# Kernel optimization log

Hardware: AMD Instinct MI355X
Metric: run time of the kernel (lower is better)

Reference implementation:

```python
import jax, jax.numpy as jnp
import numpy as np

B, M, N, D = 16, 1024, 1024, 512
DIST_THRESH = 0.3
NUM_SINK = 8


def setup_inputs() -> dict:
    key = jax.random.key(0)
    k1, k2, k3, k4 = jax.random.split(key, 4)
    return {
        "tra_feats": jax.random.normal(k1, (B, M, D), jnp.float32),
        "det_feats": jax.random.normal(k2, (B, N, D), jnp.float32),
        "tra_loc": jax.random.uniform(k3, (B, M, 2), jnp.float32),
        "det_loc": jax.random.uniform(k4, (B, N, 2), jnp.float32),
        "alpha": jnp.ones((1,), jnp.float32),
        "eplison": jnp.zeros((1,), jnp.float32),
    }


def _sinkhorn(C, log_a, log_b, lambd, num_sink):
    # log-domain unrolled Sinkhorn: P_ij = exp(log_p), marginals a (rows), b (cols)
    log_p = -C / lambd
    def step(lp, _):
        lp = lp - (jax.nn.logsumexp(lp, axis=-1, keepdims=True) - log_a[:, None])
        lp = lp - (jax.nn.logsumexp(lp, axis=-2, keepdims=True) - log_b[None, :])
        return lp, None
    log_p, _ = jax.lax.scan(step, log_p, None, length=num_sink)
    # final row normalization (standard unrolled-sinkhorn convention)
    log_p = log_p - (jax.nn.logsumexp(log_p, axis=-1, keepdims=True) - log_a[:, None])
    return jnp.exp(log_p)


def _per_graph(tf, df, tl, dl, alpha, lambd):
    n1 = jnp.linalg.norm(tf, axis=-1, keepdims=True)          # [M,1]
    n2 = jnp.linalg.norm(df, axis=-1, keepdims=True)          # [N,1]
    d2 = jnp.sum((tl[:, None, :] - dl[None, :, :]) ** 2, -1)  # [M,N] squared cdist
    mask = (jnp.sqrt(d2) <= DIST_THRESH).astype(tf.dtype)
    corr = (tf @ df.T) / (n1 * n2.T) * mask                   # masked cosine similarity
    m, n = corr.shape
    # augment with dustbin row/col filled with learnable alpha
    top = jnp.concatenate([corr, jnp.full((m, 1), alpha, corr.dtype)], axis=1)
    bot = jnp.full((1, n + 1), alpha, corr.dtype)
    couplings = jnp.concatenate([top, bot], axis=0)           # [M+1, N+1]
    norm = 1.0 / (m + n)
    a_aug = jnp.full((m + 1,), norm, corr.dtype).at[-1].set(norm * n)
    b_aug = jnp.full((n + 1,), norm, corr.dtype).at[-1].set(norm * m)
    p = _sinkhorn(1.0 - couplings, jnp.log(a_aug), jnp.log(b_aug), lambd, NUM_SINK)
    return p * (m + n)


def reference(tra_feats, det_feats, tra_loc, det_loc, alpha, eplison):
    a = alpha[0]
    lambd = jnp.exp(eplison[0]) + 0.03
    f = jax.vmap(lambda tf, df, tl, dl: _per_graph(tf, df, tl, dl, a, lambd))
    return f(tra_feats, det_feats, tra_loc, det_loc)   # [B, M+1, N+1]
```

## Files before the change

### kernel.cpp

```cpp
#include <hip/hip_runtime.h>
#include <math.h>

#define B_ 16
#define M_ 1024
#define N_ 1024
#define D_ 512
#define MP1 1025
#define NP1 1025
#define NUM_SINK 8
#define BK 64
#define SSTR 1024
#define VSTR 1028
#define NCHK 16
#define LOG_NORM (-7.6246189861593985f)
#define LOG_HALF (-0.6931471805599453f)

typedef __attribute__((ext_vector_type(8))) short bf16x8;
typedef __attribute__((ext_vector_type(4))) float f32x4;
typedef __attribute__((ext_vector_type(2))) float f32x2;

__device__ inline short f2bf(float x) {
    unsigned u = __builtin_bit_cast(unsigned, x);
    u = (u + 0x7FFFu + ((u >> 16) & 1u)) >> 16;
    return (short)u;
}

#if __has_builtin(__builtin_amdgcn_cvt_pk_fp8_f32) && __has_builtin(__builtin_amdgcn_cvt_pk_f32_fp8)
#define FP8_HW 1
#else
#define FP8_HW 0
#endif

__device__ inline unsigned char enc8(float x) {
#if FP8_HW
    return (unsigned char)(__builtin_amdgcn_cvt_pk_fp8_f32(x, x, 0, false) & 0xFF);
#else
    unsigned s = (__builtin_bit_cast(unsigned, x) >> 31) << 7;
    float ax = fminf(fabsf(x), 448.0f);
    unsigned bits;
    if (ax < 0.015625f) {
        bits = (unsigned)(ax * 512.0f + 0.5f);
        if (bits > 8) bits = 8;
    } else {
        int e; float m = frexpf(ax, &e);
        int k = e - 1;
        int j = (int)((m * 2.0f - 1.0f) * 8.0f + 0.5f);
        if (j == 8) { j = 0; k += 1; }
        if (k > 8) { k = 8; j = 7; }
        bits = ((unsigned)(k + 7) << 3) | (unsigned)j;
    }
    return (unsigned char)(s | bits);
#endif
}

__device__ inline void dec4(unsigned u, float* o) {
#if FP8_HW
    f32x2 a = __builtin_amdgcn_cvt_pk_f32_fp8((int)u, false);
    f32x2 b = __builtin_amdgcn_cvt_pk_f32_fp8((int)u, true);
    o[0] = a[0]; o[1] = a[1]; o[2] = b[0]; o[3] = b[1];
#else
    #pragma unroll
    for (int i = 0; i < 4; ++i) {
        unsigned bt = (u >> (8 * i)) & 0xFF;
        unsigned s = bt >> 7, em = bt & 0x7F;
        float mag;
        if (em >= 0x08) {
            unsigned fb = (((em >> 3) + 120) << 23) | ((em & 7) << 20);
            mag = __builtin_bit_cast(float, fb);
        } else {
            mag = (float)em * 0.001953125f;
        }
        o[i] = s ? -mag : mag;
    }
#endif
}

__device__ inline void gload16(const void* g, void* l) {
    __builtin_amdgcn_global_load_lds(
        (const __attribute__((address_space(1))) unsigned int*)g,
        (__attribute__((address_space(3))) unsigned int*)l, 16, 0, 0);
}

template<bool PRE>
__global__ __launch_bounds__(256) void norms_kernel_t(
    const float* __restrict__ tf, const float* __restrict__ df,
    float* __restrict__ inv1, float* __restrict__ inv2,
    unsigned short* __restrict__ tfh, unsigned short* __restrict__ dfh,
    float* __restrict__ v, float* __restrict__ sums_p)
{
    if (PRE && blockIdx.x == 0) {
        const int nv = B_ * VSTR, ns = 2 * B_ * 17;
        for (int t = threadIdx.x; t < nv + ns; t += 256) {
            if (t < nv) v[t] = 0.f;
            else {
                int u2 = t - nv;
                int p = u2 / (B_ * 17), s = u2 % 17;
                sums_p[u2] = (p == 0 && s == 0) ? 1025.0f : 0.f;
            }
        }
    }
    int w = (blockIdx.x * 256 + threadIdx.x) >> 6;
    int lane = threadIdx.x & 63;
    if (w >= B_ * 2048) return;
    int b = w >> 11;
    int rr = w & 2047;
    const float* src;
    float* dst = nullptr;
    unsigned short* dsth = nullptr;
    if (rr < M_) { src = tf + ((size_t)b * M_ + rr) * D_;
                   if (!PRE) dst = inv1 + b * M_ + rr;
                   if (PRE)  dsth = tfh + ((size_t)b * M_ + rr) * D_; }
    else         { src = df + ((size_t)b * N_ + (rr - M_)) * D_;
                   if (!PRE) dst = inv2 + b * N_ + (rr - M_);
                   if (PRE)  dsth = dfh + ((size_t)b * N_ + (rr - M_)) * D_; }
    float4 x = *(const float4*)(src + lane * 4);
    float4 y = *(const float4*)(src + 256 + lane * 4);
    float ss = x.x*x.x + x.y*x.y + x.z*x.z + x.w*x.w
             + y.x*y.x + y.y*y.y + y.z*y.z + y.w*y.w;
    #pragma unroll
    for (int o = 32; o; o >>= 1) ss += __shfl_xor(ss, o);
    if (PRE) {
        float rn = rsqrtf(ss);
        ushort4 hx, hy;
        hx.x = (unsigned short)f2bf(x.x*rn); hx.y = (unsigned short)f2bf(x.y*rn);
        hx.z = (unsigned short)f2bf(x.z*rn); hx.w = (unsigned short)f2bf(x.w*rn);
        hy.x = (unsigned short)f2bf(y.x*rn); hy.y = (unsigned short)f2bf(y.y*rn);
        hy.z = (unsigned short)f2bf(y.z*rn); hy.w = (unsigned short)f2bf(y.w*rn);
        *(ushort4*)(dsth + lane * 4) = hx;
        *(ushort4*)(dsth + 256 + lane * 4) = hy;
    } else {
        if (lane == 0) *dst = 1.0f / sqrtf(ss);
    }
}

template<int MODE>
__global__ __launch_bounds__(256) void gemm_s_kernel(
    const void* __restrict__ A, const void* __restrict__ Bm,
    const float* __restrict__ tl, const float* __restrict__ dl,
    const float* __restrict__ inv1, const float* __restrict__ inv2,
    const float* __restrict__ eps_p, void* __restrict__ Sout)
{
    __shared__ __align__(16) unsigned short As[2][128 * BK];
    __shared__ __align__(16) unsigned short Bs[2][128 * BK];

    int flat = blockIdx.x;
    int swz = (flat & 7) * 128 + (flat >> 3);
    int jb = swz & 7, ib = (swz >> 3) & 7;
    int b  = swz >> 6;
    int i0 = ib * 128;
    int j0 = jb * 128;

    int tid  = threadIdx.x;
    int lane = tid & 63;
    int w    = tid >> 6;
    int wm   = w >> 1, wn = w & 1;

    f32x4 acc[4][4] = {};

    if constexpr (MODE == 2) {
        const unsigned short* Ah = (const unsigned short*)A  + (size_t)b * M_ * D_;
        const unsigned short* Bh = (const unsigned short*)Bm + (size_t)b * N_ * D_;
        int gcol = ((lane & 7) ^ (lane >> 3)) << 3;
        int rloc = lane >> 3;

        auto stage = [&](int k0, int buf) {
            #pragma unroll
            for (int c = 0; c < 4; ++c) {
                int r = (w * 4 + c) * 8 + rloc;
                gload16(Ah + (size_t)(i0 + r) * D_ + k0 + gcol,
                        (char*)As[buf] + (w * 4 + c) * 1024 + lane * 16);
                gload16(Bh + (size_t)(j0 + r) * D_ + k0 + gcol,
                        (char*)Bs[buf] + (w * 4 + c) * 1024 + lane * 16);
            }
        };

        stage(0, 0);
        __syncthreads();
        int cur = 0;
        for (int t = 0; t < D_ / BK; ++t) {
            if (t < D_ / BK - 1) stage((t + 1) * BK, cur ^ 1);
            #pragma unroll
            for (int ks = 0; ks < 2; ++ks) {
                int kb = ks * 64 + ((lane >> 4) << 4);
                bf16x8 af[4], bfr[4];
                #pragma unroll
                for (int m = 0; m < 4; ++m) {
                    int ra = wm * 64 + m * 16 + (lane & 15);
                    af[m] = *(const bf16x8*)((const char*)As[cur] + ra * 128 + (kb ^ ((ra & 7) << 4)));
                    int rb = wn * 64 + m * 16 + (lane & 15);
                    bfr[m] = *(const bf16x8*)((const char*)Bs[cur] + rb * 128 + (kb ^ ((rb & 7) << 4)));
                }
                #pragma unroll
                for (int m = 0; m < 4; ++m)
                    #pragma unroll
                    for (int n = 0; n < 4; ++n)
                        acc[m][n] = __builtin_amdgcn_mfma_f32_16x16x32_bf16(af[m], bfr[n], acc[m][n], 0, 0, 0);
            }
            __syncthreads();
            cur ^= 1;
        }
    } else {
        const float* Ab = (const float*)A  + (size_t)b * M_ * D_;
        const float* Bb = (const float*)Bm + (size_t)b * N_ * D_;
        int seg   = tid & 7;
        int rbase = tid >> 3;
        for (int k0 = 0; k0 < D_; k0 += BK) {
            #pragma unroll
            for (int rr = 0; rr < 4; ++rr) {
                int r = rbase + rr * 32;
                int colx = (seg * 16) ^ ((r & 7) << 4);
                {
                    const float* pa = Ab + (size_t)(i0 + r) * D_ + k0 + seg * 8;
                    float4 a0 = *(const float4*)pa;
                    float4 a1 = *(const float4*)(pa + 4);
                    bf16x8 hv;
                    hv[0] = f2bf(a0.x); hv[1] = f2bf(a0.y); hv[2] = f2bf(a0.z); hv[3] = f2bf(a0.w);
                    hv[4] = f2bf(a1.x); hv[5] = f2bf(a1.y); hv[6] = f2bf(a1.z); hv[7] = f2bf(a1.w);
                    *(bf16x8*)((char*)As[0] + r * 128 + colx) = hv;
                }
                {
                    const float* pb = Bb + (size_t)(j0 + r) * D_ + k0 + seg * 8;
                    float4 b0 = *(const float4*)pb;
                    float4 b1 = *(const float4*)(pb + 4);
                    bf16x8 hv;
                    hv[0] = f2bf(b0.x); hv[1] = f2bf(b0.y); hv[2] = f2bf(b0.z); hv[3] = f2bf(b0.w);
                    hv[4] = f2bf(b1.x); hv[5] = f2bf(b1.y); hv[6] = f2bf(b1.z); hv[7] = f2bf(b1.w);
                    *(bf16x8*)((char*)Bs[0] + r * 128 + colx) = hv;
                }
            }
            __syncthreads();
            #pragma unroll
            for (int ks = 0; ks < 2; ++ks) {
                int kb = ks * 64 + ((lane >> 4) << 4);
                bf16x8 af[4], bfr[4];
                #pragma unroll
                for (int m = 0; m < 4; ++m) {
                    int ra = wm * 64 + m * 16 + (lane & 15);
                    af[m] = *(const bf16x8*)((const char*)As[0] + ra * 128 + (kb ^ ((ra & 7) << 4)));
                    int rb = wn * 64 + m * 16 + (lane & 15);
                    bfr[m] = *(const bf16x8*)((const char*)Bs[0] + rb * 128 + (kb ^ ((rb & 7) << 4)));
                }
                #pragma unroll
                for (int m = 0; m < 4; ++m)
                    #pragma unroll
                    for (int n = 0; n < 4; ++n)
                        acc[m][n] = __builtin_amdgcn_mfma_f32_16x16x32_bf16(af[m], bfr[n], acc[m][n], 0, 0, 0);
            }
            __syncthreads();
        }
    }

    float lam = __expf(eps_p[0]) + 0.03f;
    float inv_lam = 1.0f / lam;
    int crow0 = i0 + wm * 64;
    int ccol0 = j0 + wn * 64;
    int rlane = lane >> 4;
    int clane = lane & 15;

    float invb_[4], dlx_[4], dly_[4];
    #pragma unroll
    for (int n = 0; n < 4; ++n) {
        int j = ccol0 + n * 16 + clane;
        if (MODE != 2) invb_[n] = inv2[b * N_ + j];
        dlx_[n]  = dl[((size_t)b * N_ + j) * 2 + 0];
        dly_[n]  = dl[((size_t)b * N_ + j) * 2 + 1];
    }
    #pragma unroll
    for (int m = 0; m < 4; ++m) {
        #pragma unroll
        for (int reg = 0; reg < 4; ++reg) {
            int i = crow0 + m * 16 + rlane * 4 + reg;
            float inva = (MODE != 2) ? inv1[b * M_ + i] : 1.0f;
            float tlx  = tl[((size_t)b * M_ + i) * 2 + 0];
            float tly  = tl[((size_t)b * M_ + i) * 2 + 1];
            #pragma unroll
            for (int n = 0; n < 4; ++n) {
                float cosv = (MODE == 2) ? acc[m][n][reg]
                                         : acc[m][n][reg] * inva * invb_[n];
                float dx = tlx - dlx_[n];
                float dy = tly - dly_[n];
                float mi = (fmaf(dx, dx, dy * dy) <= 0.09f) ? inv_lam : 0.0f;
                float val = fmaf(cosv, mi, -inv_lam);
                int col = ccol0 + n * 16 + clane;
                if (MODE >= 1) {
                    unsigned char* Srow = (unsigned char*)Sout + ((size_t)b * M_ + i) * SSTR;
                    Srow[col] = enc8(val);
                } else {
                    float* Srow = (float*)Sout + ((size_t)b * MP1 + i) * NP1;
                    Srow[col] = val;
                }
            }
        }
    }
}

__global__ __launch_bounds__(256) void init_hv(
    float* __restrict__ v, float* __restrict__ sums_p)
{
    int t = blockIdx.x * 256 + threadIdx.x;
    if (t < B_ * VSTR) v[t] = 0.f;
    int u2 = t - B_ * VSTR;
    if (u2 >= 0 && u2 < 2 * B_ * 17) {
        int p = u2 / (B_ * 17), s = u2 % 17;
        sums_p[u2] = (p == 0 && s == 0) ? 1025.0f : 0.f;
    }
}

__global__ __launch_bounds__(256, 1) void rowcol64(
    const unsigned char* __restrict__ Sh, const float* __restrict__ v,
    float* __restrict__ ps,
    const float* __restrict__ alpha_p, const float* __restrict__ eps_p)
{
    int blk = blockIdx.x;
    int b = blk >> 4, k = blk & 15;
    int tid = threadIdx.x, lane = tid & 63, w = tid >> 6;

    __shared__ float red[4][64][17];

    const float* vb = v + (size_t)b * VSTR;
    float vreg[16];
    {
        float4 v0 = *(const float4*)(vb + lane * 8);
        float4 v1 = *(const float4*)(vb + lane * 8 + 4);
        float4 v2 = *(const float4*)(vb + 512 + lane * 8);
        float4 v3 = *(const float4*)(vb + 512 + lane * 8 + 4);
        vreg[0]=v0.x; vreg[1]=v0.y; vreg[2]=v0.z; vreg[3]=v0.w;
        vreg[4]=v1.x; vreg[5]=v1.y; vreg[6]=v1.z; vreg[7]=v1.w;
        vreg[8]=v2.x; vreg[9]=v2.y; vreg[10]=v2.z; vreg[11]=v2.w;
        vreg[12]=v3.x; vreg[13]=v3.y; vreg[14]=v3.z; vreg[15]=v3.w;
    }
    float lam = __expf(eps_p[0]) + 0.03f;
    float s_a = (alpha_p[0] - 1.0f) / lam;
    float et16c = __expf(s_a + vb[1024]);

    const unsigned char* Sb = Sh + ((size_t)b << 20);
    int rbase = k * 64 + w * 16;

    uint2 g0[16], g1[16];
    #pragma unroll
    for (int rr = 0; rr < 16; ++rr) {
        const unsigned char* row = Sb + (size_t)(rbase + rr) * SSTR;
        g0[rr] = *(const uint2*)(row + lane * 8);
        g1[rr] = *(const uint2*)(row + 512 + lane * 8);
    }

    float creg[16] = {};
    float sum_scale = 0.f;

    #pragma unroll
    for (int rr = 0; rr < 16; ++rr) {
        float d0[8], d1[8];
        dec4(g0[rr].x, d0); dec4(g0[rr].y, d0 + 4);
        dec4(g1[rr].x, d1); dec4(g1[rr].y, d1 + 4);
        float et[16];
        float rs = 0.f;
        #pragma unroll
        for (int e = 0; e < 8; ++e) { et[e] = __expf(d0[e] + vreg[e]); rs += et[e]; }
        #pragma unroll
        for (int e = 0; e < 8; ++e) { et[8+e] = __expf(d1[e] + vreg[8+e]); rs += et[8+e]; }
        #pragma unroll
        for (int o = 32; o; o >>= 1) rs += __shfl_xor(rs, o);
        rs += et16c;
        float scale = (1.0f / 2048.0f) / rs;
        #pragma unroll
        for (int e = 0; e < 16; ++e) creg[e] += et[e] * scale;
        sum_scale += scale;
    }

    #pragma unroll
    for (int e = 0; e < 16; ++e) red[w][lane][e] = creg[e];
    if (lane == 0) red[w][0][16] = sum_scale;
    __syncthreads();

    float* pso = ps + (size_t)(k * 16 + b) * 1025;
    for (int j = tid; j < 1024; j += 256) {
        int lane_j = (j & 511) >> 3;
        int e_j    = ((j >> 9) << 3) | (j & 7);
        pso[j] = red[0][lane_j][e_j] + red[1][lane_j][e_j]
               + red[2][lane_j][e_j] + red[3][lane_j][e_j];
    }
    if (tid == 0)
        pso[1024] = et16c * (red[0][0][16] + red[1][0][16] + red[2][0][16] + red[3][0][16]);
}

__global__ __launch_bounds__(256) void colpass32(
    const float* __restrict__ ps, float* __restrict__ v,
    float* __restrict__ sums_p, int it)
{
    int gw = blockIdx.x * 4 + (threadIdx.x >> 6);
    int lane = threadIdx.x & 63;
    if (gw >= B_ * 17) return;
    int b = gw / 17, seg = gw % 17;
    int j = seg * 64 + lane;
    int par = it & 1;
    float sum_old = 0.f;
    #pragma unroll
    for (int s = 0; s < 17; ++s) sum_old += sums_p[par * (B_ * 17) + b * 17 + s];
    float ev = 0.f;
    if (j <= 1024) {
        size_t vidx = (size_t)b * VSTR + j;
        float vj = v[vidx];
        const float* pp = ps + (size_t)b * 1025 + j;
        float cs = 0.f;
        #pragma unroll
        for (int c = 0; c < NCHK; ++c) cs += pp[(size_t)c * (16 * 1025)];
        cs += 0.5f * __expf(vj) / sum_old;
        float lb = (j == 1024) ? LOG_HALF : LOG_NORM;
        float vn = vj + lb - __logf(cs);
        v[vidx] = vn;
        ev = __expf(vn);
    }
    #pragma unroll
    for (int o = 32; o; o >>= 1) ev += __shfl_xor(ev, o);
    if (lane == 0) sums_p[(par ^ 1) * (B_ * 17) + b * 17 + seg] = ev;
}

__global__ __launch_bounds__(256) void final32(
    const unsigned char* __restrict__ Sh, const float* __restrict__ v,
    const float* __restrict__ sums_p,
    const float* __restrict__ alpha_p, const float* __restrict__ eps_p,
    float* __restrict__ out)
{
    int blk = blockIdx.x;
    int tid = threadIdx.x, lane = tid & 63, w = tid >> 6;

    if (blk >= 512) {
        int gw = (blk - 512) * 4 + w;
        if (gw >= B_ * 17) return;
        int b = gw / 17, seg = gw % 17, j = seg * 64 + lane;
        if (j > 1024) return;
        float sumv = 0.f;
        int par = NUM_SINK & 1;
        #pragma unroll
        for (int s = 0; s < 17; ++s) sumv += sums_p[par * (B_ * 17) + b * 17 + s];
        out[((size_t)b * MP1 + 1024) * NP1 + j] = __expf(v[(size_t)b * VSTR + j]) * 1024.0f / sumv;
        return;
    }

    int b = blk >> 5, k = blk & 31;
    const float* vb = v + (size_t)b * VSTR;
    float vreg[16];
    {
        float4 v0 = *(const float4*)(vb + lane * 8);
        float4 v1 = *(const float4*)(vb + lane * 8 + 4);
        float4 v2 = *(const float4*)(vb + 512 + lane * 8);
        float4 v3 = *(const float4*)(vb + 512 + lane * 8 + 4);
        vreg[0]=v0.x; vreg[1]=v0.y; vreg[2]=v0.z; vreg[3]=v0.w;
        vreg[4]=v1.x; vreg[5]=v1.y; vreg[6]=v1.z; vreg[7]=v1.w;
        vreg[8]=v2.x; vreg[9]=v2.y; vreg[10]=v2.z; vreg[11]=v2.w;
        vreg[12]=v3.x; vreg[13]=v3.y; vreg[14]=v3.z; vreg[15]=v3.w;
    }
    float lam = __expf(eps_p[0]) + 0.03f;
    float s_a = (alpha_p[0] - 1.0f) / lam;
    float et16c = __expf(s_a + vb[1024]);

    const unsigned char* Sb = Sh + ((size_t)b << 20);
    int rbase = k * 32 + w * 8;

    #pragma unroll
    for (int g = 0; g < 2; ++g) {
        uint2 g0[4], g1[4];
        #pragma unroll
        for (int rr = 0; rr < 4; ++rr) {
            const unsigned char* row = Sb + (size_t)(rbase + g * 4 + rr) * SSTR;
            g0[rr] = *(const uint2*)(row + lane * 8);
            g1[rr] = *(const uint2*)(row + 512 + lane * 8);
        }
        #pragma unroll
        for (int rr = 0; rr < 4; ++rr) {
            int r = rbase + g * 4 + rr;
            float d0[8], d1[8];
            dec4(g0[rr].x, d0); dec4(g0[rr].y, d0 + 4);
            dec4(g1[rr].x, d1); dec4(g1[rr].y, d1 + 4);
            float et[16];
            float rs = 0.f;
            #pragma unroll
            for (int e = 0; e < 8; ++e) { et[e] = __expf(d0[e] + vreg[e]); rs += et[e]; }
            #pragma unroll
            for (int e = 0; e < 8; ++e) { et[8+e] = __expf(d1[e] + vreg[8+e]); rs += et[8+e]; }
            #pragma unroll
            for (int o = 32; o; o >>= 1) rs += __shfl_xor(rs, o);
            rs += et16c;
            float sc = 1.0f / rs;
            float* orow = out + ((size_t)b * MP1 + r) * NP1;
            float4 o0 = {et[0]*sc,  et[1]*sc,  et[2]*sc,  et[3]*sc};
            float4 o1 = {et[4]*sc,  et[5]*sc,  et[6]*sc,  et[7]*sc};
            float4 o2 = {et[8]*sc,  et[9]*sc,  et[10]*sc, et[11]*sc};
            float4 o3 = {et[12]*sc, et[13]*sc, et[14]*sc, et[15]*sc};
            *(float4*)(orow + lane * 8)           = o0;
            *(float4*)(orow + lane * 8 + 4)       = o1;
            *(float4*)(orow + 512 + lane * 8)     = o2;
            *(float4*)(orow + 512 + lane * 8 + 4) = o3;
            if (lane == 0) orow[1024] = et16c * sc;
        }
    }
}


__global__ __launch_bounds__(256) void fill_edges_f32(
    float* __restrict__ Sout, const float* __restrict__ alpha_p, const float* __restrict__ eps_p)
{
    int t = blockIdx.x * 256 + threadIdx.x;
    if (t >= B_ * (NP1 + M_)) return;
    int b = t / (NP1 + M_), r = t % (NP1 + M_);
    float lam = expf(eps_p[0]) + 0.03f;
    float s = (alpha_p[0] - 1.0f) / lam;
    size_t idx;
    if (r < NP1) idx = ((size_t)b * MP1 + M_) * NP1 + r;
    else         idx = ((size_t)b * MP1 + (r - NP1)) * NP1 + N_;
    Sout[idx] = s;
}

__global__ __launch_bounds__(256) void row_pass_kernel(
    const float* __restrict__ S, const float* __restrict__ v, float* __restrict__ u)
{
    int w = (blockIdx.x * 256 + threadIdx.x) >> 6;
    int lane = threadIdx.x & 63;
    if (w >= B_ * MP1) return;
    int b = w / MP1, i = w % MP1;
    const float* row = S + ((size_t)b * MP1 + i) * NP1;
    const float* vb = v + b * NP1;
    float sm = 0.f;
    #pragma unroll
    for (int q = 0; q < 17; ++q) {
        int j = lane + q * 64;
        if (j < NP1) sm += expf(row[j] + vb[j]);
    }
    #pragma unroll
    for (int o = 32; o; o >>= 1) sm += __shfl_xor(sm, o);
    if (lane == 0) {
        float la = (i == M_) ? LOG_HALF : LOG_NORM;
        u[b * MP1 + i] = la - logf(sm);
    }
}

__global__ __launch_bounds__(256) void col_pass1_kernel(
    const float* __restrict__ S, const float* __restrict__ u,
    float* __restrict__ pm, float* __restrict__ ps)
{
    int j = blockIdx.x * 256 + threadIdx.x;
    int b = blockIdx.z;
    int i0 = blockIdx.y * 128;
    int i1 = min(i0 + 128, MP1);
    if (j >= NP1) return;
    const float* p  = S + ((size_t)b * MP1 + i0) * NP1 + j;
    const float* ub = u + b * MP1;
    float sm = 0.f;
    for (int i = i0; i < i1; ++i) {
        sm += expf(*p + ub[i]);
        p += NP1;
    }
    int idx = (blockIdx.y * B_ + b) * NP1 + j;
    pm[idx] = 0.f;
    ps[idx] = sm;
}

__global__ __launch_bounds__(256) void col_pass2_kernel(
    const float* __restrict__ pm, const float* __restrict__ ps, float* __restrict__ v)
{
    int j = blockIdx.x * 256 + threadIdx.x;
    int b = blockIdx.y;
    if (j >= NP1) return;
    float Ssum = 0.f;
    #pragma unroll
    for (int c = 0; c < 9; ++c) Ssum += ps[(c * B_ + b) * NP1 + j];
    float lb = (j == N_) ? LOG_HALF : LOG_NORM;
    v[b * NP1 + j] = lb - logf(Ssum);
}

__global__ __launch_bounds__(256) void row_final_kernel(
    float* __restrict__ S, const float* __restrict__ v)
{
    int w = (blockIdx.x * 256 + threadIdx.x) >> 6;
    int lane = threadIdx.x & 63;
    if (w >= B_ * MP1) return;
    int b = w / MP1, i = w % MP1;
    float* row = S + ((size_t)b * MP1 + i) * NP1;
    const float* vb = v + b * NP1;
    float et[17];
    float sm = 0.f;
    #pragma unroll
    for (int q = 0; q < 17; ++q) {
        int j = lane + q * 64;
        float e = 0.f;
        if (j < NP1) e = expf(row[j] + vb[j]);
        et[q] = e;
        sm += e;
    }
    #pragma unroll
    for (int o = 32; o; o >>= 1) sm += __shfl_xor(sm, o);
    float A = (i == M_) ? 0.5f : (1.0f / 2048.0f);
    float scale = (A / sm) * 2048.0f;
    #pragma unroll
    for (int q = 0; q < 17; ++q) {
        int j = lane + q * 64;
        if (j < NP1) row[j] = et[q] * scale;
    }
}

__global__ __launch_bounds__(256) void zero_kernel(float* __restrict__ p, int n)
{
    int i = blockIdx.x * 256 + threadIdx.x;
    if (i < n) p[i] = 0.f;
}

extern "C" void kernel_launch(void* const* d_in, const int* in_sizes, int n_in,
                              void* d_out, int out_size, void* d_ws, size_t ws_size,
                              hipStream_t stream)
{
    const float* tf    = (const float*)d_in[0];
    const float* df    = (const float*)d_in[1];
    const float* tl    = (const float*)d_in[2];
    const float* dl    = (const float*)d_in[3];
    const float* alpha = (const float*)d_in[4];
    const float* eps   = (const float*)d_in[5];
    float* out = (float*)d_out;

    const size_t bf_one   = (size_t)B_ * M_ * D_ * 2;
    const size_t sh_bytes = (size_t)B_ * M_ * SSTR;
    const size_t vf       = (size_t)B_ * VSTR;
    const size_t sums_f   = 2 * B_ * 17;
    const size_t invs_f   = (size_t)B_ * M_ * 2;
    const size_t need_pre = 2 * bf_one + sh_bytes + (vf + sums_f) * 4 + 512;
    const size_t need_mid = sh_bytes + (vf + sums_f + invs_f) * 4 + 512;

    int initblocks = (int)((vf + sums_f + 255) / 256);

    if (ws_size >= need_pre) {
        unsigned short* tfh = (unsigned short*)d_ws;
        unsigned short* dfh = tfh + (size_t)B_ * M_ * D_;
        unsigned char* Sh = (unsigned char*)d_ws + 2 * bf_one;
        float* fbase = (float*)((char*)d_ws + ((2 * bf_one + sh_bytes + 255) & ~(size_t)255));
        float* v      = fbase;
        float* sums_p = v + vf;
        float* ps     = out;

        norms_kernel_t<true><<<(B_ * 2048) / 4, 256, 0, stream>>>(tf, df, nullptr, nullptr, tfh, dfh, v, sums_p);
        gemm_s_kernel<2><<<1024, 256, 0, stream>>>(tfh, dfh, tl, dl, nullptr, nullptr, eps, Sh);

        for (int it = 0; it < NUM_SINK; ++it) {
            rowcol64<<<256, 256, 0, stream>>>(Sh, v, ps, alpha, eps);
            colpass32<<<68, 256, 0, stream>>>(ps, v, sums_p, it);
        }
        final32<<<580, 256, 0, stream>>>(Sh, v, sums_p, alpha, eps, out);
    } else if (ws_size >= need_mid) {
        unsigned char* Sh = (unsigned char*)d_ws;
        float* fbase = (float*)((char*)d_ws + ((sh_bytes + 255) & ~(size_t)255));
        float* inv1   = fbase;
        float* inv2   = inv1 + B_ * M_;
        float* v      = inv2 + B_ * N_;
        float* sums_p = v + vf;
        float* ps     = out;

        init_hv<<<initblocks, 256, 0, stream>>>(v, sums_p);
        norms_kernel_t<false><<<(B_ * 2048) / 4, 256, 0, stream>>>(tf, df, inv1, inv2, nullptr, nullptr, nullptr, nullptr);
        gemm_s_kernel<1><<<1024, 256, 0, stream>>>(tf, df, tl, dl, inv1, inv2, eps, Sh);

        for (int it = 0; it < NUM_SINK; ++it) {
            rowcol64<<<256, 256, 0, stream>>>(Sh, v, ps, alpha, eps);
            colpass32<<<68, 256, 0, stream>>>(ps, v, sums_p, it);
        }
        final32<<<580, 256, 0, stream>>>(Sh, v, sums_p, alpha, eps, out);
    } else {
        float* S = out;
        float* ws = (float*)d_ws;
        float* inv1 = ws;
        float* inv2 = inv1 + B_ * M_;
        float* u    = inv2 + B_ * N_;
        float* v    = u + B_ * MP1;
        float* pm   = v + B_ * NP1;
        float* ps   = pm + 9 * B_ * NP1;

        zero_kernel<<<(B_ * NP1 + 255) / 256, 256, 0, stream>>>(v, B_ * NP1);
        norms_kernel_t<false><<<(B_ * 2048) / 4, 256, 0, stream>>>(tf, df, inv1, inv2, nullptr, nullptr, nullptr, nullptr);
        gemm_s_kernel<0><<<1024, 256, 0, stream>>>(tf, df, tl, dl, inv1, inv2, eps, S);
        fill_edges_f32<<<(B_ * (NP1 + M_) + 255) / 256, 256, 0, stream>>>(S, alpha, eps);

        int rowblocks = (B_ * MP1 + 3) / 4;
        for (int it = 0; it < NUM_SINK; ++it) {
            row_pass_kernel<<<rowblocks, 256, 0, stream>>>(S, v, u);
            col_pass1_kernel<<<dim3(5, 9, 16), 256, 0, stream>>>(S, u, pm, ps);
            col_pass2_kernel<<<dim3(5, 16), 256, 0, stream>>>(pm, ps, v);
        }
        row_final_kernel<<<rowblocks, 256, 0, stream>>>(S, v);
    }
}
```

Before: 145.3 us.

## Fuse column pass into rowcol kernel via last-block atomic counter

The separate colpass32 kernel is removed. Its column update now runs inside rowcol64, in the last block to finish each batch, which it detects with an atomic counter and threadfences. The per-segment partial sums array shrinks to one sum per batch. This drops 8 kernel launches and their gaps, but the column update for each batch becomes serialized on a single block, and correctness depends on the memory fences.

New measurement: 242.8 us. 1.67x slower.

```diff
diff --git a/kernel.cpp b/kernel.cpp
--- a/kernel.cpp
+++ b/kernel.cpp
@@ -86,18 +86,13 @@
     const float* __restrict__ tf, const float* __restrict__ df,
     float* __restrict__ inv1, float* __restrict__ inv2,
     unsigned short* __restrict__ tfh, unsigned short* __restrict__ dfh,
-    float* __restrict__ v, float* __restrict__ sums_p)
+    float* __restrict__ v, float* __restrict__ sums, int* __restrict__ cnt)
 {
     if (PRE && blockIdx.x == 0) {
-        const int nv = B_ * VSTR, ns = 2 * B_ * 17;
-        for (int t = threadIdx.x; t < nv + ns; t += 256) {
-            if (t < nv) v[t] = 0.f;
-            else {
-                int u2 = t - nv;
-                int p = u2 / (B_ * 17), s = u2 % 17;
-                sums_p[u2] = (p == 0 && s == 0) ? 1025.0f : 0.f;
-            }
-        }
+        const int nv = B_ * VSTR;
+        for (int t = threadIdx.x; t < nv; t += 256) v[t] = 0.f;
+        if (threadIdx.x < 2 * B_) sums[threadIdx.x] = (threadIdx.x < B_) ? 1025.0f : 0.f;
+        if (threadIdx.x < B_) cnt[threadIdx.x] = 0;
     }
     int w = (blockIdx.x * 256 + threadIdx.x) >> 6;
     int lane = threadIdx.x & 63;
@@ -295,27 +290,28 @@
 }
 
 __global__ __launch_bounds__(256) void init_hv(
-    float* __restrict__ v, float* __restrict__ sums_p)
+    float* __restrict__ v, float* __restrict__ sums, int* __restrict__ cnt)
 {
     int t = blockIdx.x * 256 + threadIdx.x;
     if (t < B_ * VSTR) v[t] = 0.f;
-    int u2 = t - B_ * VSTR;
-    if (u2 >= 0 && u2 < 2 * B_ * 17) {
-        int p = u2 / (B_ * 17), s = u2 % 17;
-        sums_p[u2] = (p == 0 && s == 0) ? 1025.0f : 0.f;
+    if (blockIdx.x == 0) {
+        if (threadIdx.x < 2 * B_) sums[threadIdx.x] = (threadIdx.x < B_) ? 1025.0f : 0.f;
+        if (threadIdx.x < B_) cnt[threadIdx.x] = 0;
     }
 }
 
 __global__ __launch_bounds__(256, 1) void rowcol64(
-    const unsigned char* __restrict__ Sh, const float* __restrict__ v,
-    float* __restrict__ ps,
-    const float* __restrict__ alpha_p, const float* __restrict__ eps_p)
+    const unsigned char* __restrict__ Sh, float* __restrict__ v,
+    float* __restrict__ ps, float* __restrict__ sums, int* __restrict__ cnt,
+    const float* __restrict__ alpha_p, const float* __restrict__ eps_p, int it)
 {
     int blk = blockIdx.x;
     int b = blk >> 4, k = blk & 15;
     int tid = threadIdx.x, lane = tid & 63, w = tid >> 6;
 
     __shared__ float red[4][64][17];
+    __shared__ int lastf;
+    __shared__ float evred[4];
 
     const float* vb = v + (size_t)b * VSTR;
     float vreg[16];
@@ -381,43 +377,54 @@
     }
     if (tid == 0)
         pso[1024] = et16c * (red[0][0][16] + red[1][0][16] + red[2][0][16] + red[3][0][16]);
-}
-
-__global__ __launch_bounds__(256) void colpass32(
-    const float* __restrict__ ps, float* __restrict__ v,
-    float* __restrict__ sums_p, int it)
-{
-    int gw = blockIdx.x * 4 + (threadIdx.x >> 6);
-    int lane = threadIdx.x & 63;
-    if (gw >= B_ * 17) return;
-    int b = gw / 17, seg = gw % 17;
-    int j = seg * 64 + lane;
-    int par = it & 1;
-    float sum_old = 0.f;
-    #pragma unroll
-    for (int s = 0; s < 17; ++s) sum_old += sums_p[par * (B_ * 17) + b * 17 + s];
-    float ev = 0.f;
-    if (j <= 1024) {
-        size_t vidx = (size_t)b * VSTR + j;
-        float vj = v[vidx];
-        const float* pp = ps + (size_t)b * 1025 + j;
+
+    if (tid == 0) {
+        __threadfence();
+        lastf = (atomicAdd(&cnt[b], 1) == 15);
+    }
+    __syncthreads();
+    if (!lastf) return;
+    __threadfence();
+
+    float sum_old = sums[(it & 1) * B_ + b];
+    const float* pb_ = ps + (size_t)b * 1025;
+    float* vout = v + (size_t)b * VSTR;
+    float ev_acc = 0.f;
+    #pragma unroll
+    for (int q = 0; q < 4; ++q) {
+        int j = tid + q * 256;
+        float vj = vout[j];
         float cs = 0.f;
         #pragma unroll
-        for (int c = 0; c < NCHK; ++c) cs += pp[(size_t)c * (16 * 1025)];
+        for (int c = 0; c < NCHK; ++c) cs += pb_[(size_t)c * (B_ * 1025) + j];
         cs += 0.5f * __expf(vj) / sum_old;
-        float lb = (j == 1024) ? LOG_HALF : LOG_NORM;
-        float vn = vj + lb - __logf(cs);
-        v[vidx] = vn;
-        ev = __expf(vn);
-    }
-    #pragma unroll
-    for (int o = 32; o; o >>= 1) ev += __shfl_xor(ev, o);
-    if (lane == 0) sums_p[(par ^ 1) * (B_ * 17) + b * 17 + seg] = ev;
+        float vn = vj + LOG_NORM - __logf(cs);
+        vout[j] = vn;
+        ev_acc += __expf(vn);
+    }
+    if (tid == 0) {
+        float vj = vout[1024];
+        float cs = 0.f;
+        #pragma unroll
+        for (int c = 0; c < NCHK; ++c) cs += pb_[(size_t)c * (B_ * 1025) + 1024];
+        cs += 0.5f * __expf(vj) / sum_old;
+        float vn = vj + LOG_HALF - __logf(cs);
+        vout[1024] = vn;
+        ev_acc += __expf(vn);
+    }
+    #pragma unroll
+    for (int o = 32; o; o >>= 1) ev_acc += __shfl_xor(ev_acc, o);
+    if (lane == 0) evred[w] = ev_acc;
+    __syncthreads();
+    if (tid == 0) {
+        sums[((it + 1) & 1) * B_ + b] = evred[0] + evred[1] + evred[2] + evred[3];
+        cnt[b] = 0;
+    }
 }
 
 __global__ __launch_bounds__(256) void final32(
     const unsigned char* __restrict__ Sh, const float* __restrict__ v,
-    const float* __restrict__ sums_p,
+    const float* __restrict__ sums,
     const float* __restrict__ alpha_p, const float* __restrict__ eps_p,
     float* __restrict__ out)
 {
@@ -429,10 +436,7 @@
         if (gw >= B_ * 17) return;
         int b = gw / 17, seg = gw % 17, j = seg * 64 + lane;
         if (j > 1024) return;
-        float sumv = 0.f;
-        int par = NUM_SINK & 1;
-        #pragma unroll
-        for (int s = 0; s < 17; ++s) sumv += sums_p[par * (B_ * 17) + b * 17 + s];
+        float sumv = sums[(NUM_SINK & 1) * B_ + b];
         out[((size_t)b * MP1 + 1024) * NP1 + j] = __expf(v[(size_t)b * VSTR + j]) * 1024.0f / sumv;
         return;
     }
@@ -619,48 +623,45 @@
     const size_t bf_one   = (size_t)B_ * M_ * D_ * 2;
     const size_t sh_bytes = (size_t)B_ * M_ * SSTR;
     const size_t vf       = (size_t)B_ * VSTR;
-    const size_t sums_f   = 2 * B_ * 17;
+    const size_t sums_f   = 2 * B_;
+    const size_t cnt_i    = B_;
     const size_t invs_f   = (size_t)B_ * M_ * 2;
-    const size_t need_pre = 2 * bf_one + sh_bytes + (vf + sums_f) * 4 + 512;
-    const size_t need_mid = sh_bytes + (vf + sums_f + invs_f) * 4 + 512;
-
-    int initblocks = (int)((vf + sums_f + 255) / 256);
+    const size_t need_pre = 2 * bf_one + sh_bytes + (vf + sums_f + cnt_i) * 4 + 512;
+    const size_t need_mid = sh_bytes + (vf + sums_f + cnt_i + invs_f) * 4 + 512;
 
     if (ws_size >= need_pre) {
         unsigned short* tfh = (unsigned short*)d_ws;
         unsigned short* dfh = tfh + (size_t)B_ * M_ * D_;
         unsigned char* Sh = (unsigned char*)d_ws + 2 * bf_one;
         float* fbase = (float*)((char*)d_ws + ((2 * bf_one + sh_bytes + 255) & ~(size_t)255));
-        float* v      = fbase;
-        float* sums_p = v + vf;
-        float* ps     = out;
-
-        norms_kernel_t<true><<<(B_ * 2048) / 4, 256, 0, stream>>>(tf, df, nullptr, nullptr, tfh, dfh, v, sums_p);
+        float* v    = fbase;
+        float* sums = v + vf;
+        int*   cnt  = (int*)(sums + sums_f);
+        float* ps   = out;
+
+        norms_kernel_t<true><<<(B_ * 2048) / 4, 256, 0, stream>>>(tf, df, nullptr, nullptr, tfh, dfh, v, sums, cnt);
         gemm_s_kernel<2><<<1024, 256, 0, stream>>>(tfh, dfh, tl, dl, nullptr, nullptr, eps, Sh);
 
-        for (int it = 0; it < NUM_SINK; ++it) {
-            rowcol64<<<256, 256, 0, stream>>>(Sh, v, ps, alpha, eps);
-            colpass32<<<68, 256, 0, stream>>>(ps, v, sums_p, it);
-        }
-        final32<<<580, 256, 0, stream>>>(Sh, v, sums_p, alpha, eps, out);
+        for (int it = 0; it < NUM_SINK; ++it)
+            rowcol64<<<256, 256, 0, stream>>>(Sh, v, ps, sums, cnt, alpha, eps, it);
+        final32<<<512 + 68, 256, 0, stream>>>(Sh, v, sums, alpha, eps, out);
     } else if (ws_size >= need_mid) {
         unsigned char* Sh = (unsigned char*)d_ws;
         float* fbase = (float*)((char*)d_ws + ((sh_bytes + 255) & ~(size_t)255));
-        float* inv1   = fbase;
-        float* inv2   = inv1 + B_ * M_;
-        float* v      = inv2 + B_ * N_;
-        float* sums_p = v + vf;
-        float* ps     = out;
-
-        init_hv<<<initblocks, 256, 0, stream>>>(v, sums_p);
-        norms_kernel_t<false><<<(B_ * 2048) / 4, 256, 0, stream>>>(tf, df, inv1, inv2, nullptr, nullptr, nullptr, nullptr);
+        float* inv1 = fbase;
+        float* inv2 = inv1 + B_ * M_;
+        float* v    = inv2 + B_ * N_;
+        float* sums = v + vf;
+        int*   cnt  = (int*)(sums + sums_f);
+        float* ps   = out;
+
+        init_hv<<<(int)((vf + 255) / 256), 256, 0, stream>>>(v, sums, cnt);
+        norms_kernel_t<false><<<(B_ * 2048) / 4, 256, 0, stream>>>(tf, df, inv1, inv2, nullptr, nullptr, nullptr, nullptr, nullptr);
         gemm_s_kernel<1><<<1024, 256, 0, stream>>>(tf, df, tl, dl, inv1, inv2, eps, Sh);
 
-        for (int it = 0; it < NUM_SINK; ++it) {
-            rowcol64<<<256, 256, 0, stream>>>(Sh, v, ps, alpha, eps);
-            colpass32<<<68, 256, 0, stream>>>(ps, v, sums_p, it);
-        }
-        final32<<<580, 256, 0, stream>>>(Sh, v, sums_p, alpha, eps, out);
+        for (int it = 0; it < NUM_SINK; ++it)
+            rowcol64<<<256, 256, 0, stream>>>(Sh, v, ps, sums, cnt, alpha, eps, it);
+        final32<<<512 + 68, 256, 0, stream>>>(Sh, v, sums, alpha, eps, out);
     } else {
         float* S = out;
         float* ws = (float*)d_ws;
@@ -672,7 +673,7 @@
         float* ps   = pm + 9 * B_ * NP1;
 
         zero_kernel<<<(B_ * NP1 + 255) / 256, 256, 0, stream>>>(v, B_ * NP1);
-        norms_kernel_t<false><<<(B_ * 2048) / 4, 256, 0, stream>>>(tf, df, inv1, inv2, nullptr, nullptr, nullptr, nullptr);
+        norms_kernel_t<false><<<(B_ * 2048) / 4, 256, 0, stream>>>(tf, df, inv1, inv2, nullptr, nullptr, nullptr, nullptr, nullptr);
         gemm_s_kernel<0><<<1024, 256, 0, stream>>>(tf, df, tl, dl, inv1, inv2, eps, S);
         fill_edges_f32<<<(B_ * (NP1 + M_) + 255) / 256, 256, 0, stream>>>(S, alpha, eps);
 
```
